# Kernel optimization log

Hardware: AMD Instinct MI355X
Metric: run time of the kernel (lower is better)

The kernel has to match this reference:

```python
import math
import jax, jax.numpy as jnp
import numpy as np

B, T, C, H = 4, 1024, 1024, 16
HD = C // H
BLOCK = 1024


def setup_inputs() -> dict:
    key = jax.random.key(0)
    k0, k1, k2, k3 = jax.random.split(key, 4)
    x = jax.random.normal(k0, (B, T, C), dtype=jnp.float32)
    # torch Linear weight is (out, in); we store (in, out) and apply x @ W + b
    W_attn = jax.random.normal(k1, (C, 3 * C), dtype=jnp.float32) * 0.02
    b_attn = jnp.zeros((3 * C,), dtype=jnp.float32)
    W_proj = jax.random.normal(k2, (C, C), dtype=jnp.float32) * 0.02
    b_proj = jnp.zeros((C,), dtype=jnp.float32)
    # rel_pos_emb: (n_head, block_size, head_dim), std 0.02 (leading 1 dim dropped)
    rel_pos_emb = jax.random.normal(k3, (H, BLOCK, HD), dtype=jnp.float32) * 0.02
    return {"x": x, "W_attn": W_attn, "b_attn": b_attn,
            "W_proj": W_proj, "b_proj": b_proj, "rel_pos_emb": rel_pos_emb}


def reference(x, W_attn, b_attn, W_proj, b_proj, rel_pos_emb):
    Bx, Tx, Cx = x.shape
    qkv = x @ W_attn + b_attn                      # (B, T, 3C)
    q, k, v = jnp.split(qkv, 3, axis=2)
    q = q.reshape(Bx, Tx, H, HD).transpose(0, 2, 1, 3)   # (B, H, T, hd)
    k = k.reshape(Bx, Tx, H, HD).transpose(0, 2, 1, 3)
    v = v.reshape(Bx, Tx, H, HD).transpose(0, 2, 1, 3)

    att = jnp.einsum('bhid,bhjd->bhij', q, k)      # (B, H, T, T)

    # relative position score: pos[b,h,i,j] = sum_d E[h, clamp(i-j,0), d] * k[b,h,j,d]
    # compute P[b,h,r,j] = <E[h,r,:], k[b,h,j,:]> then gather r = clamp(i-j, 0)
    rng = jnp.arange(Tx)
    dist = jnp.clip(rng[:, None] - rng[None, :], 0, None)          # (T, T)
    P = jnp.einsum('hrd,bhjd->bhrj', rel_pos_emb[:, :Tx], k)       # (B, H, T, T)
    pos_score = jnp.take_along_axis(P, dist[None, None, :, :], axis=2)
    att = att + pos_score

    att = att * (1.0 / math.sqrt(HD))
    causal = jnp.tril(jnp.ones((Tx, Tx), dtype=bool))
    att = jnp.where(causal[None, None], att, -jnp.inf)
    att = jax.nn.softmax(att, axis=-1)
    # dropout p=0.0 -> identity
    y = jnp.einsum('bhij,bhjd->bhid', att, v)      # (B, H, T, hd)
    y = y.transpose(0, 2, 1, 3).reshape(Bx, Tx, Cx)
    return y @ W_proj + b_proj
```

## Files before the change

### kernel.cpp

```cpp
#include <hip/hip_runtime.h>


typedef __bf16 bf16x8 __attribute__((ext_vector_type(8)));
typedef float f32x4 __attribute__((ext_vector_type(4)));
typedef unsigned short ushort_t;

#define T_SEQ 1024
#define NHEAD 16
#define HDIM 64
#define PLANE 4194304
#define C1SCALE 0.1803368836f
#define SMAX 20.0f

__device__ __forceinline__ float bf2f(ushort_t h) {
    unsigned int u = ((unsigned int)h) << 16;
    float f; __builtin_memcpy(&f, &u, 4); return f;
}
__device__ __forceinline__ ushort_t f2bf(float f) {
    __bf16 h = (__bf16)f;
    ushort_t u; __builtin_memcpy(&u, &h, 2); return u;
}

__global__ __launch_bounds__(256) void sentinel_kernel(float* out, int n, float val) {
    const int i = blockIdx.x * 256 + threadIdx.x;
    if (i < n) out[i] = val;
}

__global__ __launch_bounds__(256) void prep(
    const float* __restrict__ x, ushort_t* __restrict__ x16,
    const float* __restrict__ E, ushort_t* __restrict__ E16,
    const float* __restrict__ Wa, ushort_t* __restrict__ WaT,
    const float* __restrict__ Wp, ushort_t* __restrict__ WpT)
{
    __shared__ ushort_t t[64][65];
    const int bid = blockIdx.x;
    if (bid < 5120) {
        const float* src; ushort_t* dst; int base; float sc;
        if (bid < 4096) { src = x; dst = x16; base = bid * 1024; sc = 1.0f; }
        else            { src = E; dst = E16; base = (bid - 4096) * 1024; sc = C1SCALE; }
        const int i = base + (int)threadIdx.x * 4;
        const float4 v = *reinterpret_cast<const float4*>(src + i);
        union { unsigned long long u; ushort_t s[4]; } o;
        o.s[0] = f2bf(v.x * sc); o.s[1] = f2bf(v.y * sc);
        o.s[2] = f2bf(v.z * sc); o.s[3] = f2bf(v.w * sc);
        *reinterpret_cast<unsigned long long*>(dst + i) = o.u;
        return;
    }
    const float* W; ushort_t* Wt; int Kdim, Ndim, n0, k0;
    if (bid < 5888) {
        const int r = bid - 5120;
        W = Wa; Wt = WaT; Kdim = 1024; Ndim = 3072;
        n0 = (r % 48) * 64; k0 = (r / 48) * 64;
    } else {
        const int r = bid - 5888;
        W = Wp; Wt = WpT; Kdim = 1024; Ndim = 1024;
        n0 = (r % 16) * 64; k0 = (r / 16) * 64;
    }
    const int cx = threadIdx.x & 63, ry = threadIdx.x >> 6;
#pragma unroll
    for (int i = 0; i < 16; i++) {
        const int r = ry + i * 4;
        t[r][cx] = f2bf(W[(size_t)(k0 + r) * Ndim + n0 + cx]);
    }
    __syncthreads();
#pragma unroll
    for (int i = 0; i < 16; i++) {
        const int r = ry + i * 4;
        Wt[(size_t)(n0 + r) * Kdim + k0 + cx] = t[cx][r];
    }
}

template <int MODE, int BN>
__global__ __launch_bounds__(256) void gemm128(
    const ushort_t* __restrict__ A16, const ushort_t* __restrict__ Bt,
    const float* __restrict__ bias, void* __restrict__ out_,
    int Ndim, int Kdim)
{
    constexpr int NT = BN / 32;
    __shared__ __align__(16) ushort_t As[128 * 32];
    __shared__ __align__(16) ushort_t Bs[BN * 32];

    const int tid = threadIdx.x;
    const int w = tid >> 6;
    const int lane = tid & 63;
    const int l15 = lane & 15;
    const int quad = lane >> 4;
    const int m0 = blockIdx.y * 128, n0 = blockIdx.x * BN;
    const int wm = (w & 1) * 64, wn = (w >> 1) * (BN / 2);

    f32x4 acc[4][NT];
#pragma unroll
    for (int mt = 0; mt < 4; mt++)
#pragma unroll
        for (int nt = 0; nt < NT; nt++) acc[mt][nt] = (f32x4){0.f, 0.f, 0.f, 0.f};

    for (int kk = 0; kk < Kdim; kk += 32) {
        __syncthreads();
#pragma unroll
        for (int t = 0; t < 2; t++) {
            const int chunk = w * 128 + t * 64 + lane;
            const int row = chunk >> 2, kc = (chunk & 3) * 8;
            __builtin_amdgcn_global_load_lds(
                (const __attribute__((address_space(1))) void*)
                    (A16 + (size_t)(m0 + row) * Kdim + kk + kc),
                (__attribute__((address_space(3))) void*)
                    (As + (size_t)(w * 128 + t * 64) * 8), 16, 0, 0);
            if (BN == 128)
                __builtin_amdgcn_global_load_lds(
                    (const __attribute__((address_space(1))) void*)
                        (Bt + (size_t)(n0 + row) * Kdim + kk + kc),
                    (__attribute__((address_space(3))) void*)
                        (Bs + (size_t)(w * 128 + t * 64) * 8), 16, 0, 0);
        }
        if (BN == 64) {
            const int chunk = w * 64 + lane;
            const int row = chunk >> 2, kc = (chunk & 3) * 8;
            __builtin_amdgcn_global_load_lds(
                (const __attribute__((address_space(1))) void*)
                    (Bt + (size_t)(n0 + row) * Kdim + kk + kc),
                (__attribute__((address_space(3))) void*)
                    (Bs + (size_t)(w * 64) * 8), 16, 0, 0);
        }
        __syncthreads();

        bf16x8 af[4], bf[NT];
#pragma unroll
        for (int mt = 0; mt < 4; mt++)
            af[mt] = *reinterpret_cast<const bf16x8*>(&As[(wm + mt * 16 + l15) * 32 + quad * 8]);
#pragma unroll
        for (int nt = 0; nt < NT; nt++)
            bf[nt] = *reinterpret_cast<const bf16x8*>(&Bs[(wn + nt * 16 + l15) * 32 + quad * 8]);
#pragma unroll
        for (int mt = 0; mt < 4; mt++)
#pragma unroll
            for (int nt = 0; nt < NT; nt++)
                acc[mt][nt] = __builtin_amdgcn_mfma_f32_16x16x32_bf16(
                    af[mt], bf[nt], acc[mt][nt], 0, 0, 0);
    }

#pragma unroll
    for (int mt = 0; mt < 4; mt++)
#pragma unroll
        for (int nt = 0; nt < NT; nt++) {
            const int n = n0 + wn + nt * 16 + l15;
            const float bv = bias[n];
#pragma unroll
            for (int r = 0; r < 4; r++) {
                const int m = m0 + wm + mt * 16 + quad * 4 + r;
                const float val = acc[mt][nt][r] + bv;
                if (MODE == 0) {
                    ushort_t* ws = (ushort_t*)out_;
                    const int which = n >> 10;
                    const int cc = n & 1023;
                    const int h = cc >> 6, d = cc & 63;
                    const int bb = m >> 10, t = m & 1023;
                    if (which == 2) {
                        ws[2 * PLANE + ((size_t)(bb * NHEAD + h) * HDIM + d) * T_SEQ + t] = f2bf(val);
                    } else {
                        const float sv = (which == 0) ? val * C1SCALE : val;
                        ws[(size_t)which * PLANE +
                           ((size_t)(bb * NHEAD + h) * T_SEQ + t) * HDIM + d] = f2bf(sv);
                    }
                } else {
                    ((float*)out_)[(size_t)m * Ndim + n] = val;
                }
            }
        }
}

__global__ __launch_bounds__(256) void flash_attn(
    const ushort_t* __restrict__ qp, const ushort_t* __restrict__ kp,
    const ushort_t* __restrict__ vTp, const ushort_t* __restrict__ E16,
    ushort_t* __restrict__ y16)
{
    __shared__ __align__(16) ushort_t Ks[64 * 64];
    __shared__ __align__(16) ushort_t Vt[64 * 64];
    __shared__ __align__(16) ushort_t Es[128 * 64];
    __shared__ __align__(16) ushort_t Ps[64 * 64];

    const int bh = blockIdx.x;
    const int h = bh & (NHEAD - 1);
    const int b = bh >> 4;
    const int it = 15 - (int)blockIdx.y;
    const int tid = threadIdx.x;
    const int w = tid >> 6;
    const int lane = tid & 63;
    const int l15 = lane & 15;
    const int quad = lane >> 4;

    const size_t base = (size_t)bh * T_SEQ * HDIM;
    const ushort_t* Eh = E16 + (size_t)h * T_SEQ * HDIM;
    const ushort_t* vTb = vTp + (size_t)bh * 65536;

    const int kswz = (l15 & 7) << 3;
    const int jswz = quad << 4;

    const int srow = lane >> 3;
    const int scc  = lane & 7;

    bf16x8 ones;
#pragma unroll
    for (int i = 0; i < 8; i++) ones[i] = (__bf16)1.0f;

    const int i0 = it * 64;

    bf16x8 qf[2];
    {
        const ushort_t* qrow = qp + base + (size_t)(i0 + w * 16 + l15) * HDIM;
        qf[0] = *reinterpret_cast<const bf16x8*>(qrow + quad * 8);
        qf[1] = *reinterpret_cast<const bf16x8*>(qrow + 32 + quad * 8);
    }

    f32x4 o[4], o5;
#pragma unroll
    for (int dt = 0; dt < 4; dt++) o[dt] = (f32x4){0.f, 0.f, 0.f, 0.f};
    o5 = (f32x4){0.f, 0.f, 0.f, 0.f};

    for (int j0 = 0; j0 <= i0; j0 += 64) {
        const int d0 = i0 - j0;
        __syncthreads();
        {
#pragma unroll
            for (int t = 0; t < 2; t++) {
                const int r0 = w * 16 + t * 8;
                const int row = r0 + srow;
                const int sx = (scc ^ (row & 7)) << 3;
                __builtin_amdgcn_global_load_lds(
                    (const __attribute__((address_space(1))) void*)
                        (kp + base + (size_t)(j0 + row) * HDIM + sx),
                    (__attribute__((address_space(3))) void*)(&Ks[r0 * 64]),
                    16, 0, 0);
                __builtin_amdgcn_global_load_lds(
                    (const __attribute__((address_space(1))) void*)
                        (vTb + (size_t)row * T_SEQ + j0 + sx),
                    (__attribute__((address_space(3))) void*)(&Vt[r0 * 64]),
                    16, 0, 0);
            }
#pragma unroll
            for (int t = 0; t < 4; t++) {
                const int r0 = w * 32 + t * 8;
                const int row = r0 + srow;
                int g = d0 - 64 + row;
                g = g < 0 ? 0 : (g > 1023 ? 1023 : g);
                const int sx = (scc ^ (row & 7)) << 3;
                __builtin_amdgcn_global_load_lds(
                    (const __attribute__((address_space(1))) void*)
                        (Eh + (size_t)g * HDIM + sx),
                    (__attribute__((address_space(3))) void*)(&Es[r0 * 64]),
                    16, 0, 0);
            }
        }
        __syncthreads();

        f32x4 s[4], pb[2][4];
#pragma unroll
        for (int nt = 0; nt < 4; nt++) {
            s[nt] = (f32x4){0.f, 0.f, 0.f, 0.f};
            pb[0][nt] = (f32x4){0.f, 0.f, 0.f, 0.f};
            pb[1][nt] = (f32x4){0.f, 0.f, 0.f, 0.f};
        }
        __builtin_amdgcn_s_setprio(1);
#pragma unroll
        for (int ks = 0; ks < 2; ks++) {
            const int ko = ks * 32 + quad * 8;
            const bf16x8 ae0 = *reinterpret_cast<const bf16x8*>(&Es[(w * 32 + l15) * 64 + (ko ^ kswz)]);
            const bf16x8 ae1 = *reinterpret_cast<const bf16x8*>(&Es[(w * 32 + 16 + l15) * 64 + (ko ^ kswz)]);
#pragma unroll
            for (int nt = 0; nt < 4; nt++) {
                const bf16x8 bk = *reinterpret_cast<const bf16x8*>(&Ks[(nt * 16 + l15) * 64 + (ko ^ kswz)]);
                s[nt] = __builtin_amdgcn_mfma_f32_16x16x32_bf16(qf[ks], bk, s[nt], 0, 0, 0);
                pb[0][nt] = __builtin_amdgcn_mfma_f32_16x16x32_bf16(ae0, bk, pb[0][nt], 0, 0, 0);
                pb[1][nt] = __builtin_amdgcn_mfma_f32_16x16x32_bf16(ae1, bk, pb[1][nt], 0, 0, 0);
            }
        }
        __builtin_amdgcn_s_setprio(0);
#pragma unroll
        for (int mf = 0; mf < 2; mf++)
#pragma unroll
            for (int nt = 0; nt < 4; nt++) {
                const int jl = nt * 16 + l15;
#pragma unroll
                for (int r = 0; r < 4; r++) {
                    const int br = w * 32 + mf * 16 + quad * 4 + r;
                    const int il_t = br - 64 + jl;
                    if ((unsigned)il_t < 64u)
                        Ps[il_t * 64 + (jl ^ (((il_t >> 2) & 3) << 4))] = f2bf(pb[mf][nt][r]);
                }
            }
        __syncthreads();

        float pv[4][4];
        const int il0 = w * 16 + quad * 4;
        if (j0 < i0) {
#pragma unroll
            for (int nt = 0; nt < 4; nt++) {
                const int jl = nt * 16 + l15;
#pragma unroll
                for (int r = 0; r < 4; r++) {
                    const float sv = s[nt][r] + bf2f(Ps[(il0 + r) * 64 + (jl ^ jswz)]);
                    pv[nt][r] = exp2f(sv - SMAX);
                }
            }
        } else {
#pragma unroll
            for (int nt = 0; nt < 4; nt++) {
                const int jl = nt * 16 + l15;
#pragma unroll
                for (int r = 0; r < 4; r++) {
                    const int il = il0 + r;
                    float sv = s[nt][r] + bf2f(Ps[il * 64 + (jl ^ jswz)]);
                    if (jl > il) sv = -3e38f;
                    pv[nt][r] = exp2f(sv - SMAX);
                }
            }
        }
#pragma unroll
        for (int nt = 0; nt < 4; nt++)
#pragma unroll
            for (int r = 0; r < 4; r++) {
                const int rr = w * 16 + quad * 4 + r;
                Ks[rr * 64 + ((nt * 16 + l15) ^ ((rr & 7) << 3))] = f2bf(pv[nt][r]);
            }

        __builtin_amdgcn_s_setprio(1);
#pragma unroll
        for (int ks = 0; ks < 2; ks++) {
            const int ko = ks * 32 + quad * 8;
            const bf16x8 ap = *reinterpret_cast<const bf16x8*>(&Ks[(w * 16 + l15) * 64 + (ko ^ kswz)]);
#pragma unroll
            for (int dt = 0; dt < 4; dt++) {
                const bf16x8 bv = *reinterpret_cast<const bf16x8*>(&Vt[(dt * 16 + l15) * 64 + (ko ^ kswz)]);
                o[dt] = __builtin_amdgcn_mfma_f32_16x16x32_bf16(ap, bv, o[dt], 0, 0, 0);
            }
            o5 = __builtin_amdgcn_mfma_f32_16x16x32_bf16(ap, ones, o5, 0, 0, 0);
        }
        __builtin_amdgcn_s_setprio(0);
    }

    float inv[4];
#pragma unroll
    for (int r = 0; r < 4; r++) inv[r] = 1.0f / o5[r];
#pragma unroll
    for (int dt = 0; dt < 4; dt++)
#pragma unroll
        for (int r = 0; r < 4; r++) {
            const int il = w * 16 + quad * 4 + r;
            const int d = dt * 16 + l15;
            y16[((size_t)(b * T_SEQ + i0 + il)) * 1024 + h * 64 + d] = f2bf(o[dt][r] * inv[r]);
        }
}

extern "C" void kernel_launch(void* const* d_in, const int* in_sizes, int n_in,
                              void* d_out, int out_size, void* d_ws, size_t ws_size,
                              hipStream_t stream) {
    float* out = (float*)d_out;

    const void* x = nullptr; const void* Wa = nullptr; const void* ba = nullptr;
    const void* Wp = nullptr; const void* bp = nullptr; const void* E = nullptr;
    int anomaly = 0;
    if (n_in != 6) {
        anomaly = 2;
    } else {
        int c1M = 0;
        for (int i = 0; i < 6; i++) {
            const int s = in_sizes[i];
            if      (s == 4194304) x  = d_in[i];
            else if (s == 3145728) Wa = d_in[i];
            else if (s == 3072)    ba = d_in[i];
            else if (s == 1024)    bp = d_in[i];
            else if (s == 1048576) { if (c1M == 0) Wp = d_in[i]; else E = d_in[i]; c1M++; }
            else anomaly = 1;
        }
        if (!x || !Wa || !ba || !Wp || !bp || !E || c1M != 2) anomaly = 1;
    }
    if (!anomaly && out_size != 4194304) anomaly = 3;
    if (!anomaly && ws_size < (size_t)52428800) anomaly = 4;
    if (anomaly) {
        sentinel_kernel<<<(out_size + 255) / 256, 256, 0, stream>>>(out, out_size, 1000.0f * anomaly);
        return;
    }

    ushort_t* ws   = (ushort_t*)d_ws;
    ushort_t* qp   = ws;
    ushort_t* kp   = ws + (size_t)PLANE;
    ushort_t* vTp  = ws + (size_t)2 * PLANE;
    ushort_t* y16  = ws + (size_t)3 * PLANE;
    ushort_t* x16  = ws + (size_t)4 * PLANE;
    ushort_t* WaT  = ws + (size_t)5 * PLANE;
    ushort_t* WpT  = WaT + (size_t)3145728;
    ushort_t* E16  = WpT + (size_t)1048576;

    prep<<<6144, 256, 0, stream>>>((const float*)x, x16, (const float*)E, E16,
                                   (const float*)Wa, WaT, (const float*)Wp, WpT);

    gemm128<0, 128><<<dim3(24, 32), 256, 0, stream>>>(x16, WaT, (const float*)ba, (void*)ws, 3072, 1024);

    flash_attn<<<dim3(64, 16), 256, 0, stream>>>(qp, kp, vTp, E16, y16);

    gemm128<1, 64><<<dim3(16, 32), 256, 0, stream>>>(y16, WpT, (const float*)bp, (void*)out, 1024, 1024);
}
```

Baseline: 202.9 us.

## Split long causal query tiles across two blocks with atomic partial reduction

Query tiles 8-15 in the attention kernel are split into two halves along the key dimension, each handled by its own block. The grid grows from 16 to 24 tiles per head, ordered by a lookup table. Split halves add unnormalised outputs and row sums into fp32 scratch with atomics, and a new normalisation kernel writes them back as bf16. The aim is to even out per-block causal work and shorten the tail. In exchange it adds a zeroing kernel, a normalise kernel, scratch traffic and atomic contention, and it relies on the fixed max shift so partial softmax sums can simply be added.

```diff
diff --git a/kernel.cpp b/kernel.cpp
--- a/kernel.cpp
+++ b/kernel.cpp
@@ -70,6 +70,31 @@
     }
 }
 
+__global__ __launch_bounds__(256) void zero_ws(float* __restrict__ y32,
+                                               float* __restrict__ den)
+{
+    const int bid = blockIdx.x;
+    float4* p = (bid < 2048)
+        ? reinterpret_cast<float4*>(y32) + (size_t)bid * 256 + threadIdx.x
+        : reinterpret_cast<float4*>(den) + (size_t)(bid - 2048) * 256 + threadIdx.x;
+    *p = (float4){0.f, 0.f, 0.f, 0.f};
+}
+
+__global__ __launch_bounds__(256) void norm_y(const float* __restrict__ y32,
+                                              const float* __restrict__ den,
+                                              ushort_t* __restrict__ y16)
+{
+    const int bid = blockIdx.x;
+    const int b = bid >> 9, irel = bid & 511;
+    const float4 v = reinterpret_cast<const float4*>(y32 + (size_t)bid * 1024)[threadIdx.x];
+    const float inv = 1.0f / den[(size_t)bid * 16 + (threadIdx.x >> 4)];
+    union { unsigned long long u; ushort_t s[4]; } o;
+    o.s[0] = f2bf(v.x * inv); o.s[1] = f2bf(v.y * inv);
+    o.s[2] = f2bf(v.z * inv); o.s[3] = f2bf(v.w * inv);
+    reinterpret_cast<unsigned long long*>(
+        y16 + ((size_t)(b * T_SEQ + 512 + irel)) * 1024)[threadIdx.x] = o.u;
+}
+
 template <int MODE, int BN>
 __global__ __launch_bounds__(256) void gemm128(
     const ushort_t* __restrict__ A16, const ushort_t* __restrict__ Bt,
@@ -171,17 +196,29 @@
 __global__ __launch_bounds__(256) void flash_attn(
     const ushort_t* __restrict__ qp, const ushort_t* __restrict__ kp,
     const ushort_t* __restrict__ vTp, const ushort_t* __restrict__ E16,
-    ushort_t* __restrict__ y16)
+    ushort_t* __restrict__ y16, float* __restrict__ y32,
+    float* __restrict__ den)
 {
     __shared__ __align__(16) ushort_t Ks[64 * 64];
     __shared__ __align__(16) ushort_t Vt[64 * 64];
     __shared__ __align__(16) ushort_t Es[128 * 64];
     __shared__ __align__(16) ushort_t Ps[64 * 64];
 
+    static const signed char TBL_IT[24] =
+        {15,15,14, 7,14,13,13,12, 6,12,11,11,10, 5,10, 9, 9, 8, 4, 8, 3, 2, 1, 0};
+    static const signed char TBL_HF[24] =
+        { 0, 1, 0, 2, 1, 0, 1, 0, 2, 1, 0, 1, 0, 2, 1, 0, 1, 0, 2, 1, 2, 2, 2, 2};
+
     const int bh = blockIdx.x;
     const int h = bh & (NHEAD - 1);
     const int b = bh >> 4;
-    const int it = 15 - (int)blockIdx.y;
+    const int by = blockIdx.y;
+    const int it = TBL_IT[by];
+    const int hf = TBL_HF[by];
+    const int ntile = it + 1;
+    const int jb = (hf == 1) ? ((it + 2) >> 1) : 0;
+    const int je = (hf == 0) ? ((it + 2) >> 1) : ntile;
+
     const int tid = threadIdx.x;
     const int w = tid >> 6;
     const int lane = tid & 63;
@@ -216,7 +253,8 @@
     for (int dt = 0; dt < 4; dt++) o[dt] = (f32x4){0.f, 0.f, 0.f, 0.f};
     o5 = (f32x4){0.f, 0.f, 0.f, 0.f};
 
-    for (int j0 = 0; j0 <= i0; j0 += 64) {
+    for (int jt = jb; jt < je; ++jt) {
+        const int j0 = jt * 64;
         const int d0 = i0 - j0;
         __syncthreads();
         {
@@ -337,17 +375,37 @@
         __builtin_amdgcn_s_setprio(0);
     }
 
-    float inv[4];
-#pragma unroll
-    for (int r = 0; r < 4; r++) inv[r] = 1.0f / o5[r];
-#pragma unroll
-    for (int dt = 0; dt < 4; dt++)
-#pragma unroll
-        for (int r = 0; r < 4; r++) {
-            const int il = w * 16 + quad * 4 + r;
-            const int d = dt * 16 + l15;
-            y16[((size_t)(b * T_SEQ + i0 + il)) * 1024 + h * 64 + d] = f2bf(o[dt][r] * inv[r]);
-        }
+    if (hf == 2) {
+        float inv[4];
+#pragma unroll
+        for (int r = 0; r < 4; r++) inv[r] = 1.0f / o5[r];
+#pragma unroll
+        for (int dt = 0; dt < 4; dt++)
+#pragma unroll
+            for (int r = 0; r < 4; r++) {
+                const int il = w * 16 + quad * 4 + r;
+                const int d = dt * 16 + l15;
+                y16[((size_t)(b * T_SEQ + i0 + il)) * 1024 + h * 64 + d] =
+                    f2bf(o[dt][r] * inv[r]);
+            }
+    } else {
+        const int rb = b * 512 + (i0 - 512);
+#pragma unroll
+        for (int dt = 0; dt < 4; dt++)
+#pragma unroll
+            for (int r = 0; r < 4; r++) {
+                const int il = w * 16 + quad * 4 + r;
+                const int d = dt * 16 + l15;
+                atomicAdd(&y32[((size_t)(rb + il)) * 1024 + h * 64 + d], o[dt][r]);
+            }
+        if (l15 == 0) {
+#pragma unroll
+            for (int r = 0; r < 4; r++) {
+                const int il = w * 16 + quad * 4 + r;
+                atomicAdd(&den[(size_t)(rb + il) * 16 + h], o5[r]);
+            }
+        }
+    }
 }
 
 extern "C" void kernel_launch(void* const* d_in, const int* in_sizes, int n_in,
@@ -390,12 +448,19 @@
     ushort_t* WpT  = WaT + (size_t)3145728;
     ushort_t* E16  = WpT + (size_t)1048576;
 
+    float* y32 = (float*)x16;
+    float* den = (float*)WaT;
+
     prep<<<6144, 256, 0, stream>>>((const float*)x, x16, (const float*)E, E16,
                                    (const float*)Wa, WaT, (const float*)Wp, WpT);
 
     gemm128<0, 128><<<dim3(24, 32), 256, 0, stream>>>(x16, WaT, (const float*)ba, (void*)ws, 3072, 1024);
 
-    flash_attn<<<dim3(64, 16), 256, 0, stream>>>(qp, kp, vTp, E16, y16);
+    zero_ws<<<2080, 256, 0, stream>>>(y32, den);
+
+    flash_attn<<<dim3(64, 24), 256, 0, stream>>>(qp, kp, vTp, E16, y16, y32, den);
+
+    norm_y<<<2048, 256, 0, stream>>>(y32, den, y16);
 
     gemm128<1, 64><<<dim3(16, 32), 256, 0, stream>>>(y16, WpT, (const float*)bp, (void*)out, 1024, 1024);
 }
```

New measurement: 227.2 us. +12.0%, slower.

## Double-buffer relative-position E tiles with overlapping reuse and transpose P scratch layout

Applied to the files above, without the earlier changes.

Consecutive key tiles share half of the 128-row E window. Instead of reloading all 128 rows every iteration, each step now prefetches only the next 64 rows into a ping-pong half of the E buffer while softmax runs, and indexes the halves by iteration parity. The P scratch buffer is stored transposed with a new swizzle, so each lane fetches its four bias values with one 64-bit LDS read instead of four scalar reads. The diagonal masking is merged into a single branchless loop. The cost is more delicate synchronisation, relying on a manual lgkmcnt wait and barrier around the async global-to-LDS loads.

```diff
diff --git a/kernel.cpp b/kernel.cpp
--- a/kernel.cpp
+++ b/kernel.cpp
@@ -193,7 +193,7 @@
     const ushort_t* vTb = vTp + (size_t)bh * 65536;
 
     const int kswz = (l15 & 7) << 3;
-    const int jswz = quad << 4;
+    const int pswz = (l15 & 7) << 2;
 
     const int srow = lane >> 3;
     const int scc  = lane & 7;
@@ -203,6 +203,23 @@
     for (int i = 0; i < 8; i++) ones[i] = (__bf16)1.0f;
 
     const int i0 = it * 64;
+
+    auto stage_e = [&](int k) {
+        const int sk = k & 1;
+#pragma unroll
+        for (int t = 0; t < 2; t++) {
+            const int r0 = w * 16 + t * 8;
+            const int row = r0 + srow;
+            int g = i0 - (k + 1) * 64 + row;
+            g = g < 0 ? 0 : (g > 1023 ? 1023 : g);
+            const int sx = (scc ^ (row & 7)) << 3;
+            __builtin_amdgcn_global_load_lds(
+                (const __attribute__((address_space(1))) void*)
+                    (Eh + (size_t)g * HDIM + sx),
+                (__attribute__((address_space(3))) void*)(&Es[(sk * 64 + r0) * 64]),
+                16, 0, 0);
+        }
+    };
 
     bf16x8 qf[2];
     {
@@ -216,9 +233,14 @@
     for (int dt = 0; dt < 4; dt++) o[dt] = (f32x4){0.f, 0.f, 0.f, 0.f};
     o5 = (f32x4){0.f, 0.f, 0.f, 0.f};
 
-    for (int j0 = 0; j0 <= i0; j0 += 64) {
-        const int d0 = i0 - j0;
-        __syncthreads();
+    stage_e(-1);
+    stage_e(0);
+
+    for (int jt = 0; jt <= it; ++jt) {
+        const int j0 = jt * 64;
+        asm volatile("s_waitcnt lgkmcnt(0)" ::: "memory");
+        __builtin_amdgcn_s_barrier();
+        __builtin_amdgcn_sched_barrier(0);
         {
 #pragma unroll
             for (int t = 0; t < 2; t++) {
@@ -236,22 +258,10 @@
                     (__attribute__((address_space(3))) void*)(&Vt[r0 * 64]),
                     16, 0, 0);
             }
-#pragma unroll
-            for (int t = 0; t < 4; t++) {
-                const int r0 = w * 32 + t * 8;
-                const int row = r0 + srow;
-                int g = d0 - 64 + row;
-                g = g < 0 ? 0 : (g > 1023 ? 1023 : g);
-                const int sx = (scc ^ (row & 7)) << 3;
-                __builtin_amdgcn_global_load_lds(
-                    (const __attribute__((address_space(1))) void*)
-                        (Eh + (size_t)g * HDIM + sx),
-                    (__attribute__((address_space(3))) void*)(&Es[r0 * 64]),
-                    16, 0, 0);
-            }
         }
         __syncthreads();
 
+        const int erow = (((jt & 1) ^ (w >> 1)) << 6) + (w & 1) * 32 + l15;
         f32x4 s[4], pb[2][4];
 #pragma unroll
         for (int nt = 0; nt < 4; nt++) {
@@ -263,8 +273,8 @@
 #pragma unroll
         for (int ks = 0; ks < 2; ks++) {
             const int ko = ks * 32 + quad * 8;
-            const bf16x8 ae0 = *reinterpret_cast<const bf16x8*>(&Es[(w * 32 + l15) * 64 + (ko ^ kswz)]);
-            const bf16x8 ae1 = *reinterpret_cast<const bf16x8*>(&Es[(w * 32 + 16 + l15) * 64 + (ko ^ kswz)]);
+            const bf16x8 ae0 = *reinterpret_cast<const bf16x8*>(&Es[erow * 64 + (ko ^ kswz)]);
+            const bf16x8 ae1 = *reinterpret_cast<const bf16x8*>(&Es[(erow + 16) * 64 + (ko ^ kswz)]);
 #pragma unroll
             for (int nt = 0; nt < 4; nt++) {
                 const bf16x8 bk = *reinterpret_cast<const bf16x8*>(&Ks[(nt * 16 + l15) * 64 + (ko ^ kswz)]);
@@ -284,34 +294,31 @@
                     const int br = w * 32 + mf * 16 + quad * 4 + r;
                     const int il_t = br - 64 + jl;
                     if ((unsigned)il_t < 64u)
-                        Ps[il_t * 64 + (jl ^ (((il_t >> 2) & 3) << 4))] = f2bf(pb[mf][nt][r]);
+                        Ps[jl * 64 + (il_t ^ pswz)] = f2bf(pb[mf][nt][r]);
                 }
             }
         __syncthreads();
+
+        if (jt < it) stage_e(jt + 1);
 
         float pv[4][4];
         const int il0 = w * 16 + quad * 4;
-        if (j0 < i0) {
-#pragma unroll
-            for (int nt = 0; nt < 4; nt++) {
-                const int jl = nt * 16 + l15;
-#pragma unroll
-                for (int r = 0; r < 4; r++) {
-                    const float sv = s[nt][r] + bf2f(Ps[(il0 + r) * 64 + (jl ^ jswz)]);
-                    pv[nt][r] = exp2f(sv - SMAX);
-                }
-            }
-        } else {
-#pragma unroll
-            for (int nt = 0; nt < 4; nt++) {
-                const int jl = nt * 16 + l15;
-#pragma unroll
-                for (int r = 0; r < 4; r++) {
-                    const int il = il0 + r;
-                    float sv = s[nt][r] + bf2f(Ps[il * 64 + (jl ^ jswz)]);
-                    if (jl > il) sv = -3e38f;
-                    pv[nt][r] = exp2f(sv - SMAX);
-                }
+        const bool diag = (j0 == i0);
+#pragma unroll
+        for (int nt = 0; nt < 4; nt++) {
+            const int jl = nt * 16 + l15;
+            const unsigned long long pw =
+                *reinterpret_cast<const unsigned long long*>(&Ps[jl * 64 + (il0 ^ pswz)]);
+            const unsigned w0 = (unsigned)pw, w1 = (unsigned)(pw >> 32);
+            float p[4];
+            { unsigned u = w0 << 16;         __builtin_memcpy(&p[0], &u, 4); }
+            { unsigned u = w0 & 0xFFFF0000u; __builtin_memcpy(&p[1], &u, 4); }
+            { unsigned u = w1 << 16;         __builtin_memcpy(&p[2], &u, 4); }
+            { unsigned u = w1 & 0xFFFF0000u; __builtin_memcpy(&p[3], &u, 4); }
+#pragma unroll
+            for (int r = 0; r < 4; r++) {
+                const float e = exp2f(s[nt][r] + p[r] - SMAX);
+                pv[nt][r] = (diag && jl > il0 + r) ? 0.0f : e;
             }
         }
 #pragma unroll
```

Result: no change. 202.8 us (-0.1%).
